# Kernel tuning notes

Hardware: AMD Instinct MI355X
Metric: run time of the kernel (lower is better)

Reference implementation:

```python
import jax, jax.numpy as jnp
import numpy as np

T = 28  # MAX_SENT_LEN
NEG_SLOPE = 0.02  # LeakyReLU slope


def gru_step(x, h, Wih, Whh, bih, bhh):
    # torch GRU/GRUCell gate math, gate order (r, z, n)
    gi = x @ Wih.T + bih
    gh = h @ Whh.T + bhh
    ir, iz, inn = jnp.split(gi, 3, axis=-1)
    hr, hz, hn = jnp.split(gh, 3, axis=-1)
    r = jax.nn.sigmoid(ir + hr)
    zg = jax.nn.sigmoid(iz + hz)
    n = jnp.tanh(inn + r * hn)
    return (1.0 - zg) * n + zg * h


def setup_inputs() -> dict:
    key = jax.random.key(0)
    ks = jax.random.split(key, 24)
    V, E, H, D, L, B = 32000, 256, 512, 512, 128, 512
    s = lambda i, shape: jax.random.normal(ks[i], shape, jnp.float32) * 0.05
    return dict(
        x=jax.random.randint(ks[0], (B, T), 0, V),
        x_lens=jax.random.randint(ks[1], (B,), 1, T + 1),  # lengths in [1, 28]
        emb=s(2, (V, E)),
        enc_Wih_f=s(3, (3 * H, E)), enc_Whh_f=s(4, (3 * H, H)),
        enc_bih_f=s(5, (3 * H,)), enc_bhh_f=s(6, (3 * H,)),
        enc_Wih_b=s(7, (3 * H, E)), enc_Whh_b=s(8, (3 * H, H)),
        enc_bih_b=s(9, (3 * H,)), enc_bhh_b=s(10, (3 * H,)),
        fc1_w=s(11, (L, 2 * H)), fc1_b=s(12, (L,)),
        fc2_w=s(13, (D, L)), fc2_b=s(14, (D,)),
        dec_Wih=s(15, (3 * D, D)), dec_Whh=s(16, (3 * D, D)),
        dec_bih=s(17, (3 * D,)), dec_bhh=s(18, (3 * D,)),
        re_w=s(19, (E, D)), re_b=s(20, (E,)),
        hv_w=s(21, (V, D)), hv_b=s(22, (V,)),
    )


def reference(x, x_lens, emb, enc_Wih_f, enc_Whh_f, enc_bih_f, enc_bhh_f,
              enc_Wih_b, enc_Whh_b, enc_bih_b, enc_bhh_b,
              fc1_w, fc1_b, fc2_w, fc2_b,
              dec_Wih, dec_Whh, dec_bih, dec_bhh,
              re_w, re_b, hv_w, hv_b):
    B = x.shape[0]
    H = enc_Whh_f.shape[1]
    embedded = emb[x]                       # [B,T,E]
    xs = jnp.swapaxes(embedded, 0, 1)       # [T,B,E]

    # forward direction of the packed bidirectional GRU: output at t=len-1
    # equals hidden after len steps (padding only affects later steps)
    def fstep(h, xt):
        hn = gru_step(xt, h, enc_Wih_f, enc_Whh_f, enc_bih_f, enc_bhh_f)
        return hn, hn
    h0 = jnp.zeros((B, H), embedded.dtype)
    _, ys = jax.lax.scan(fstep, h0, xs)     # [T,B,H]

    idx = x_lens - 1
    bidx = jnp.arange(B)
    ctx_f = jnp.swapaxes(ys, 0, 1)[bidx, idx]     # [B,H]
    # backward direction processes token len-1 first with h0=0, so its
    # output at position len-1 is a single GRU step on the last valid token
    x_last = embedded[bidx, idx]                  # [B,E]
    ctx_b = gru_step(x_last, h0, enc_Wih_b, enc_Whh_b, enc_bih_b, enc_bhh_b)
    context = jnp.concatenate([ctx_f, ctx_b], axis=-1)  # [B,2H]

    z = context @ fc1_w.T + fc1_b            # [B,latent]; dropout = identity (eval)

    # decoder: tf_prob=0 -> pure recurrence; same input fc_2(z) every step,
    # initial hidden = fc_2(z)
    out0 = z @ fc2_w.T + fc2_b                # [B,D]
    def dstep(h, _):
        hn = gru_step(out0, h, dec_Wih, dec_Whh, dec_bih, dec_bhh)
        return hn, hn
    _, outs = jax.lax.scan(dstep, out0, None, length=T)  # [T,B,D]

    re_emb = outs @ re_w.T + re_b             # [T,B,E]
    re_emb = jnp.where(re_emb >= 0, re_emb, NEG_SLOPE * re_emb)
    re_emb = jnp.swapaxes(re_emb, 0, 1)       # [B,T,E]
    logits = outs @ hv_w.T + hv_b             # [T,B,V]
    return logits, z, re_emb
```

## Files before the change

### kernel.cpp

```cpp
#include <hip/hip_runtime.h>

typedef unsigned short u16;
typedef unsigned int u32;
typedef __attribute__((ext_vector_type(8))) short bf16x8;
typedef __attribute__((ext_vector_type(4))) float f32x4;

#define GLOBAL_AS __attribute__((address_space(1)))
#define LDS_AS __attribute__((address_space(3)))

__device__ __forceinline__ float b2f(u16 u) {
    union { float f; u32 i; } v; v.i = ((u32)u) << 16; return v.f;
}
__device__ __forceinline__ u16 f2b(float f) {
    union { float f; u32 i; } v; v.f = f;
    u32 i = v.i;
    u32 r = (i + 0x7FFFu + ((i >> 16) & 1u)) >> 16;
    return (u16)r;
}
__device__ __forceinline__ float sigm(float x) { return 1.f / (1.f + expf(-x)); }

struct CvtJobs {
    const float* src[9];
    u16*         dst[9];
    int          end4[9];
};
__global__ void cvt_multi(CvtJobs jobs, int total4)
{
    for (int id = blockIdx.x * 256 + threadIdx.x; id < total4;
         id += gridDim.x * 256) {
        int s = 0;
        while (id >= jobs.end4[s]) ++s;
        int base = (s == 0) ? 0 : jobs.end4[s - 1];
        int i = id - base;
        float4 v = ((const float4*)jobs.src[s])[i];
        u32 w0 = (u32)f2b(v.x) | ((u32)f2b(v.y) << 16);
        u32 w1 = (u32)f2b(v.z) | ((u32)f2b(v.w) << 16);
        ((u32*)jobs.dst[s])[i * 2]     = w0;
        ((u32*)jobs.dst[s])[i * 2 + 1] = w1;
    }
}

template<bool LEAKY, bool REMAP>
__global__ __launch_bounds__(256)
void gemm_bt(const u16* __restrict__ A, const u16* __restrict__ W,
             const float* __restrict__ bias,
             float* __restrict__ Cf, u16* __restrict__ Cb,
             int M, int N, int K)
{
    __shared__ __align__(16) u16 lA[128 * 64];
    __shared__ __align__(16) u16 lB[128 * 64];

    const int tid  = threadIdx.x;
    const int lane = tid & 63;
    const int w    = tid >> 6;
    const int wr   = w >> 1;
    const int wc   = w & 1;
    const int m0   = blockIdx.y * 128;
    const int n0   = blockIdx.x * 128;

    const int lrow = lane & 15;
    const int kgrp = lane >> 4;

    f32x4 acc[4][4] = {};

    for (int k0 = 0; k0 < K; k0 += 64) {
        #pragma unroll
        for (int s = 0; s < 4; ++s) {
            int seg = w * 4 + s;
            int g   = seg * 64 + lane;
            int row = g >> 3;
            int kk  = (g & 7) * 8;
            const u16* gA = A + (size_t)(m0 + row) * K + k0 + kk;
            const u16* gB = W + (size_t)(n0 + row) * K + k0 + kk;
            __builtin_amdgcn_global_load_lds((GLOBAL_AS const void*)gA,
                                             (LDS_AS void*)(&lA[seg * 512]), 16, 0, 0);
            __builtin_amdgcn_global_load_lds((GLOBAL_AS const void*)gB,
                                             (LDS_AS void*)(&lB[seg * 512]), 16, 0, 0);
        }
        __syncthreads();
        #pragma unroll
        for (int kk = 0; kk < 64; kk += 32) {
            bf16x8 af[4], bfr[4];
            #pragma unroll
            for (int i = 0; i < 4; ++i) {
                int ar = wr * 64 + i * 16 + lrow;
                af[i]  = *(const bf16x8*)&lA[ar * 64 + kk + kgrp * 8];
                int br = wc * 64 + i * 16 + lrow;
                bfr[i] = *(const bf16x8*)&lB[br * 64 + kk + kgrp * 8];
            }
            #pragma unroll
            for (int mi = 0; mi < 4; ++mi)
                #pragma unroll
                for (int ni = 0; ni < 4; ++ni)
                    acc[mi][ni] = __builtin_amdgcn_mfma_f32_16x16x32_bf16(
                        af[mi], bfr[ni], acc[mi][ni], 0, 0, 0);
        }
        __syncthreads();
    }

    #pragma unroll
    for (int mi = 0; mi < 4; ++mi) {
        #pragma unroll
        for (int ni = 0; ni < 4; ++ni) {
            int gcol = n0 + wc * 64 + ni * 16 + lrow;
            float bv = bias ? bias[gcol] : 0.f;
            #pragma unroll
            for (int r = 0; r < 4; ++r) {
                int grow = m0 + wr * 64 + mi * 16 + kgrp * 4 + r;
                float v = acc[mi][ni][r] + bv;
                if (LEAKY) v = (v >= 0.f) ? v : 0.02f * v;
                size_t oidx;
                if (REMAP) {
                    int bb = grow & 511, tt = grow >> 9;
                    oidx = ((size_t)bb * 28 + tt) * (size_t)N + gcol;
                } else {
                    oidx = (size_t)grow * (size_t)N + gcol;
                }
                if (Cf) Cf[oidx] = v;
                if (Cb) Cb[oidx] = f2b(v);
            }
        }
    }
}

__global__ __launch_bounds__(512)
void gemm_logits(const u16* __restrict__ A, const u16* __restrict__ W,
                 const float* __restrict__ bias, float* __restrict__ C,
                 int M, int N)
{
    constexpr int K = 512;
    __shared__ __align__(16) u16 lds[4 * 2 * 8192];

    const int tid  = threadIdx.x;
    const int lane = tid & 63;
    const int w    = tid >> 6;
    const int wr   = w >> 2;
    const int wc   = w & 3;
    const int l15  = lane & 15;
    const int kg   = lane >> 4;

    {
    }
    int id = blockIdx.x;
    int xcd = id & 7;
    int o   = id >> 3;
    int g, r;
    if (o < 840) { g = o / 56; r = o % 56; }
    else         { g = 15;     r = o - 840; }
    const int by = xcd * 7 + (r % 7);
    const int bx = g * 8 + (r / 7);
    const int m0 = by * 256;
    const int n0 = bx * 256;

    auto stage = [&](int kt, int buf) {
        #pragma unroll
        for (int ld = 0; ld < 2; ++ld) {
            int g2  = ld * 512 + tid;
            int row = g2 >> 2;
            int cp  = g2 & 3;
            int scp = cp ^ ((row >> 1) & 3);
            const u16* sA = A + (size_t)(m0 + row) * K + kt * 32 + scp * 8;
            const u16* sB = W + (size_t)(n0 + row) * K + kt * 32 + scp * 8;
            u32 dst = (u32)buf * 32768u + (u32)(ld * 512 + w * 64) * 16u;
            __builtin_amdgcn_global_load_lds((GLOBAL_AS const void*)sA,
                (LDS_AS void*)((char*)lds + dst), 16, 0, 0);
            __builtin_amdgcn_global_load_lds((GLOBAL_AS const void*)sB,
                (LDS_AS void*)((char*)lds + dst + 16384u), 16, 0, 0);
        }
    };

    f32x4 acc[8][4] = {};

    auto compute = [&](int buf) {
        const char* base = (const char*)lds + buf * 32768;
        bf16x8 a[8], b[4];
        #pragma unroll
        for (int mi = 0; mi < 8; ++mi) {
            int rr = wr * 128 + mi * 16 + l15;
            a[mi] = *(const bf16x8*)(base + rr * 64 + ((kg ^ ((rr >> 1) & 3)) << 4));
        }
        #pragma unroll
        for (int ni = 0; ni < 4; ++ni) {
            int rr = wc * 64 + ni * 16 + l15;
            b[ni] = *(const bf16x8*)(base + 16384 + rr * 64 + ((kg ^ ((rr >> 1) & 3)) << 4));
        }
        __builtin_amdgcn_s_setprio(1);
        #pragma unroll
        for (int mi = 0; mi < 8; ++mi)
            #pragma unroll
            for (int ni = 0; ni < 4; ++ni)
                acc[mi][ni] = __builtin_amdgcn_mfma_f32_16x16x32_bf16(
                    a[mi], b[ni], acc[mi][ni], 0, 0, 0);
        __builtin_amdgcn_s_setprio(0);
    };

    stage(0, 0);
    stage(1, 1);
    stage(2, 2);

    #pragma unroll 1
    for (int kt = 0; kt < 13; ++kt) {
        asm volatile("s_waitcnt vmcnt(8)" ::: "memory");
        __builtin_amdgcn_sched_barrier(0);
        __builtin_amdgcn_s_barrier();
        asm volatile("" ::: "memory");
        __builtin_amdgcn_sched_barrier(0);
        stage(kt + 3, (kt + 3) & 3);
        compute(kt & 3);
    }
    asm volatile("s_waitcnt vmcnt(8)" ::: "memory");
    __builtin_amdgcn_sched_barrier(0);
    __builtin_amdgcn_s_barrier();
    asm volatile("" ::: "memory");
    __builtin_amdgcn_sched_barrier(0);
    compute(1);
    asm volatile("s_waitcnt vmcnt(4)" ::: "memory");
    __builtin_amdgcn_sched_barrier(0);
    __builtin_amdgcn_s_barrier();
    asm volatile("" ::: "memory");
    __builtin_amdgcn_sched_barrier(0);
    compute(2);
    asm volatile("s_waitcnt vmcnt(0)" ::: "memory");
    __builtin_amdgcn_sched_barrier(0);
    __builtin_amdgcn_s_barrier();
    asm volatile("" ::: "memory");
    __builtin_amdgcn_sched_barrier(0);
    compute(3);

    #pragma unroll
    for (int ni = 0; ni < 4; ++ni) {
        int gcol = n0 + wc * 64 + ni * 16 + l15;
        float bv = bias[gcol];
        #pragma unroll
        for (int mi = 0; mi < 8; ++mi) {
            #pragma unroll
            for (int r = 0; r < 4; ++r) {
                int grow = m0 + wr * 128 + mi * 16 + kg * 4 + r;
                __builtin_nontemporal_store(acc[mi][ni][r] + bv,
                                            &C[(size_t)grow * (size_t)N + gcol]);
            }
        }
    }
}

template<bool IS_DEC>
__global__ __launch_bounds__(256)
void scan_step(const u16* __restrict__ gi,
               const u16* __restrict__ Whh,
               const float* __restrict__ bhh,
               const u16* __restrict__ hprev_b,
               const float* __restrict__ hprev_f,
               u16* __restrict__ hnext_b,
               float* __restrict__ hnext_f,
               const int* __restrict__ xlens,
               u16* __restrict__ ctx,
               u16* __restrict__ outs,
               int t)
{
    __shared__ __align__(16) u16 lB[96 * 512];
    __shared__ __align__(16) u16 lA[32 * 512];

    const int tid  = threadIdx.x;
    const int lane = tid & 63;
    const int w    = tid >> 6;
    const int rh   = w >> 1;
    const int jh   = w & 1;
    const int bc   = blockIdx.x >> 4;
    const int jc   = blockIdx.x & 15;

    const int l15 = lane & 15;
    const int kg  = lane >> 4;

    #pragma unroll
    for (int s = 0; s < 24; ++s) {
        int g    = s * 256 + tid;
        int rr   = g >> 6;
        int cp   = g & 63;
        int gate = rr >> 5;
        int c    = rr & 31;
        int whrow = gate * 512 + jc * 32 + c;
        const u16* src = Whh + (size_t)whrow * 512 + (size_t)((cp ^ (rr & 7)) * 8);
        __builtin_amdgcn_global_load_lds((GLOBAL_AS const void*)src,
            (LDS_AS void*)((char*)lB + (s * 256 + w * 64) * 16), 16, 0, 0);
    }
    #pragma unroll
    for (int s = 0; s < 8; ++s) {
        int g   = s * 256 + tid;
        int row = g >> 6;
        int cp  = g & 63;
        const u16* src = hprev_b + (size_t)(bc * 32 + row) * 512
                                 + (size_t)((cp ^ (row & 7)) * 8);
        __builtin_amdgcn_global_load_lds((GLOBAL_AS const void*)src,
            (LDS_AS void*)((char*)lA + (s * 256 + w * 64) * 16), 16, 0, 0);
    }

    const int jloc = jh * 16 + l15;
    const int j    = jc * 32 + jloc;
    const int rowb = bc * 32 + rh * 16 + kg * 4;
    const float bhr = bhh[j], bhz = bhh[512 + j], bhn = bhh[1024 + j];

    const u16* gi_t = IS_DEC ? gi : gi + (size_t)t * 512 * 1536;
    float gir[4], giz[4], gin[4], hold[4];
    int   xl[4];
    #pragma unroll
    for (int r = 0; r < 4; ++r) {
        int row = rowb + r;
        gir[r]  = b2f(gi_t[row * 1536 + j]);
        giz[r]  = b2f(gi_t[row * 1536 + 512 + j]);
        gin[r]  = b2f(gi_t[row * 1536 + 1024 + j]);
        hold[r] = hprev_f[row * 512 + j];
        if (!IS_DEC) xl[r] = xlens[row];
    }
    __syncthreads();

    f32x4 acc[3] = {};
    const int arow = rh * 16 + l15;
    #pragma unroll 4
    for (int kc = 0; kc < 16; ++kc) {
        int k2 = kc * 64 + kg * 16;
        bf16x8 a = *(const bf16x8*)((const char*)lA + arow * 1024
                                    + (k2 ^ ((arow & 7) << 4)));
        #pragma unroll
        for (int g3 = 0; g3 < 3; ++g3) {
            int rr = g3 * 32 + jloc;
            bf16x8 b = *(const bf16x8*)((const char*)lB + rr * 1024
                                        + (k2 ^ ((rr & 7) << 4)));
            acc[g3] = __builtin_amdgcn_mfma_f32_16x16x32_bf16(a, b, acc[g3], 0, 0, 0);
        }
    }

    #pragma unroll
    for (int r = 0; r < 4; ++r) {
        int row = rowb + r;
        float rg = sigm(gir[r] + acc[0][r] + bhr);
        float zg = sigm(giz[r] + acc[1][r] + bhz);
        float ng = tanhf(gin[r] + rg * (acc[2][r] + bhn));
        float hn = (1.f - zg) * ng + zg * hold[r];
        hnext_f[row * 512 + j] = hn;
        hnext_b[row * 512 + j] = f2b(hn);
        if (IS_DEC) outs[((size_t)t * 512 + row) * 512 + j] = f2b(hn);
        else if (xl[r] - 1 == t) ctx[row * 1024 + j] = f2b(hn);
    }
}

__global__ void embed_k(const int* __restrict__ x, const int* __restrict__ xlens,
                        const float* __restrict__ emb,
                        u16* __restrict__ embedded, u16* __restrict__ x_last)
{
    int id = blockIdx.x * 256 + threadIdx.x;
    if (id >= 28 * 512 * 128) return;
    int e2 = id & 127;
    int tb = id >> 7;
    int b  = tb & 511;
    int t  = tb >> 9;
    int tok = x[b * 28 + t];
    const float* src = emb + (size_t)tok * 256 + e2 * 2;
    u32 v = (u32)f2b(src[0]) | ((u32)f2b(src[1]) << 16);
    *(u32*)(embedded + (size_t)tb * 256 + e2 * 2) = v;
    if (t == xlens[b] - 1)
        *(u32*)(x_last + (size_t)b * 256 + e2 * 2) = v;
}

__global__ void ctxb_k(const float* __restrict__ gi, const float* __restrict__ bhh,
                       u16* __restrict__ ctx)
{
    int idx = blockIdx.x * 256 + threadIdx.x;
    if (idx >= 512 * 512) return;
    int b = idx >> 9, j = idx & 511;
    int base = b * 1536;
    float r = sigm(gi[base + j] + bhh[j]);
    float z = sigm(gi[base + 512 + j] + bhh[512 + j]);
    float n = tanhf(gi[base + 1024 + j] + r * bhh[1024 + j]);
    ctx[b * 1024 + 512 + j] = f2b((1.f - z) * n);
}


extern "C" void kernel_launch(void* const* d_in, const int* in_sizes, int n_in,
                              void* d_out, int out_size, void* d_ws, size_t ws_size,
                              hipStream_t stream)
{
    const int*   x      = (const int*)d_in[0];
    const int*   xlens  = (const int*)d_in[1];
    const float* emb    = (const float*)d_in[2];
    const float* Wih_f  = (const float*)d_in[3];
    const float* Whh_f  = (const float*)d_in[4];
    const float* bih_f  = (const float*)d_in[5];
    const float* bhh_f  = (const float*)d_in[6];
    const float* Wih_b  = (const float*)d_in[7];
    const float* bih_b  = (const float*)d_in[9];
    const float* bhh_b  = (const float*)d_in[10];
    const float* fc1_w  = (const float*)d_in[11];
    const float* fc1_b  = (const float*)d_in[12];
    const float* fc2_w  = (const float*)d_in[13];
    const float* fc2_b  = (const float*)d_in[14];
    const float* dWih   = (const float*)d_in[15];
    const float* dWhh   = (const float*)d_in[16];
    const float* dbih   = (const float*)d_in[17];
    const float* dbhh   = (const float*)d_in[18];
    const float* re_w   = (const float*)d_in[19];
    const float* re_b   = (const float*)d_in[20];
    const float* hv_w   = (const float*)d_in[21];
    const float* hv_b   = (const float*)d_in[22];

    float* out        = (float*)d_out;
    float* out_logits = out;
    float* out_z      = out + (size_t)28 * 512 * 32000;
    float* out_re     = out_z + 512 * 128;

    char* ws = (char*)d_ws;
    size_t off = 0;
    auto alloc = [&](size_t bytes) -> void* {
        void* p = ws + off; off += (bytes + 255) & ~(size_t)255; return p;
    };
    u16* wWihf = (u16*)alloc(1536 * 256 * 2);
    u16* wWhhf = (u16*)alloc(1536 * 512 * 2);
    u16* wWihb = (u16*)alloc(1536 * 256 * 2);
    u16* wfc1  = (u16*)alloc(128 * 1024 * 2);
    u16* wfc2  = (u16*)alloc(512 * 128 * 2);
    u16* wdWih = (u16*)alloc(1536 * 512 * 2);
    u16* wdWhh = (u16*)alloc(1536 * 512 * 2);
    u16* wre   = (u16*)alloc(256 * 512 * 2);
    u16* whv   = (u16*)alloc((size_t)32000 * 512 * 2);
    u16*   hb0    = (u16*)  alloc(512 * 512 * 2);
    u16*   hb1    = (u16*)  alloc(512 * 512 * 2);
    float* hf0    = (float*)alloc(512 * 512 * 4);
    float* hf1    = (float*)alloc(512 * 512 * 4);
    u16*   ctx    = (u16*)  alloc(512 * 1024 * 2);
    float* gi_bw  = (float*)alloc(512 * 1536 * 4);
    u16*   out_zb = (u16*)  alloc(512 * 128 * 2);
    u16*   gi_dec = (u16*)  alloc(512 * 1536 * 2);
    u16*   outsb  = (u16*)  alloc((size_t)28 * 512 * 512 * 2);

    char* ds = (char*)d_out;
    size_t doff = 0;
    auto dalloc = [&](size_t bytes) -> void* {
        void* p = ds + doff; doff += (bytes + 255) & ~(size_t)255; return p;
    };
    u16* embedded = (u16*)dalloc((size_t)28 * 512 * 256 * 2);
    u16* x_last   = (u16*)dalloc(512 * 256 * 2);
    u16* gi_f     = (u16*)dalloc((size_t)28 * 512 * 1536 * 2);

    {
        CvtJobs jobs;
        const float* s[9] = { Wih_f, Whh_f, Wih_b, fc1_w, fc2_w, dWih, dWhh, re_w, hv_w };
        u16*         d[9] = { wWihf, wWhhf, wWihb, wfc1, wfc2, wdWih, wdWhh, wre, whv };
        int          n[9] = { 1536*256, 1536*512, 1536*256, 128*1024, 512*128,
                              1536*512, 1536*512, 256*512, 32000*512 };
        int cum = 0;
        for (int i = 0; i < 9; ++i) {
            jobs.src[i] = s[i]; jobs.dst[i] = d[i];
            cum += n[i] / 4; jobs.end4[i] = cum;
        }
        cvt_multi<<<2048, 256, 0, stream>>>(jobs, cum);
    }
    hipMemsetAsync(hb0, 0, 512 * 512 * 2, stream);
    hipMemsetAsync(hf0, 0, 512 * 512 * 4, stream);

    embed_k<<<7168, 256, 0, stream>>>(x, xlens, emb, embedded, x_last);

    gemm_bt<false, false><<<dim3(12, 112), 256, 0, stream>>>(
        embedded, wWihf, bih_f, nullptr, gi_f, 14336, 1536, 256);

    gemm_bt<false, false><<<dim3(12, 4), 256, 0, stream>>>(
        x_last, wWihb, bih_b, gi_bw, nullptr, 512, 1536, 256);
    ctxb_k<<<1024, 256, 0, stream>>>(gi_bw, bhh_b, ctx);

    {
        u16*   hb[2] = { hb0, hb1 };
        float* hf[2] = { hf0, hf1 };
        for (int t = 0; t < 28; ++t) {
            int s = t & 1, d = s ^ 1;
            scan_step<false><<<256, 256, 0, stream>>>(
                gi_f, wWhhf, bhh_f, hb[s], hf[s], hb[d], hf[d],
                xlens, ctx, nullptr, t);
        }
    }

    gemm_bt<false, false><<<dim3(1, 4), 256, 0, stream>>>(
        ctx, wfc1, fc1_b, out_z, out_zb, 512, 128, 1024);

    gemm_bt<false, false><<<dim3(4, 4), 256, 0, stream>>>(
        out_zb, wfc2, fc2_b, hf0, hb0, 512, 512, 128);

    gemm_bt<false, false><<<dim3(12, 4), 256, 0, stream>>>(
        hb0, wdWih, dbih, nullptr, gi_dec, 512, 1536, 512);

    {
        u16*   hb[2] = { hb0, hb1 };
        float* hf[2] = { hf0, hf1 };
        for (int t = 0; t < 28; ++t) {
            int s = t & 1, d = s ^ 1;
            scan_step<true><<<256, 256, 0, stream>>>(
                gi_dec, wdWhh, dbhh, hb[s], hf[s], hb[d], hf[d],
                nullptr, nullptr, outsb, t);
        }
    }

    gemm_bt<true, true><<<dim3(2, 112), 256, 0, stream>>>(
        outsb, wre, re_b, out_re, nullptr, 14336, 256, 512);

    gemm_logits<<<7000, 512, 0, stream>>>(
        outsb, whv, hv_b, out_logits, 14336, 32000);
}
```

Measured before the change: 1.152 ms.

## Shrink logits GEMM tile to 128x256 and read scan Whh directly from global

The logits GEMM moves from 256x256 tiles with a 4-stage LDS ring to 128x256 tiles with a 2-stage double buffer. This cuts LDS use and registers per block so more blocks fit per CU (launch bounds set to 4), and the grid doubles to 14000 blocks. The scan step kernel stops staging the Whh slice in LDS and loads B fragments straight from global memory (L2-cached), which removes the per-step LDS fill and its 96KB footprint. The costs are lower arithmetic intensity per tile in the GEMM and uncoalesced global reads in the scan inner loop.

```diff
diff --git a/kernel.cpp b/kernel.cpp
--- a/kernel.cpp
+++ b/kernel.cpp
@@ -123,13 +123,13 @@
     }
 }
 
-__global__ __launch_bounds__(512)
+__global__ __launch_bounds__(512, 4)
 void gemm_logits(const u16* __restrict__ A, const u16* __restrict__ W,
                  const float* __restrict__ bias, float* __restrict__ C,
                  int M, int N)
 {
     constexpr int K = 512;
-    __shared__ __align__(16) u16 lds[4 * 2 * 8192];
+    __shared__ __align__(16) u16 lds[2 * 12288];
 
     const int tid  = threadIdx.x;
     const int lane = tid & 63;
@@ -139,103 +139,87 @@
     const int l15  = lane & 15;
     const int kg   = lane >> 4;
 
-    {
-    }
-    int id = blockIdx.x;
+    int id  = blockIdx.x;
     int xcd = id & 7;
     int o   = id >> 3;
     int g, r;
-    if (o < 840) { g = o / 56; r = o % 56; }
-    else         { g = 15;     r = o - 840; }
-    const int by = xcd * 7 + (r % 7);
-    const int bx = g * 8 + (r / 7);
-    const int m0 = by * 256;
+    if (o < 1680) { g = o / 112; r = o % 112; }
+    else          { g = 15;      r = o - 1680; }
+    const int by = xcd * 14 + (r % 14);
+    const int bx = g * 8 + (r / 14);
+    const int m0 = by * 128;
     const int n0 = bx * 256;
 
     auto stage = [&](int kt, int buf) {
-        #pragma unroll
-        for (int ld = 0; ld < 2; ++ld) {
-            int g2  = ld * 512 + tid;
-            int row = g2 >> 2;
-            int cp  = g2 & 3;
+        {
+            int row = tid >> 2, cp = tid & 3;
             int scp = cp ^ ((row >> 1) & 3);
             const u16* sA = A + (size_t)(m0 + row) * K + kt * 32 + scp * 8;
-            const u16* sB = W + (size_t)(n0 + row) * K + kt * 32 + scp * 8;
-            u32 dst = (u32)buf * 32768u + (u32)(ld * 512 + w * 64) * 16u;
+            u32 dst = (u32)buf * 24576u + (u32)(w * 64) * 16u;
             __builtin_amdgcn_global_load_lds((GLOBAL_AS const void*)sA,
                 (LDS_AS void*)((char*)lds + dst), 16, 0, 0);
+        }
+        #pragma unroll
+        for (int ld = 0; ld < 2; ++ld) {
+            int gch = ld * 512 + tid;
+            int row = gch >> 2, cp = gch & 3;
+            int scp = cp ^ ((row >> 1) & 3);
+            const u16* sB = W + (size_t)(n0 + row) * K + kt * 32 + scp * 8;
+            u32 dst = (u32)buf * 24576u + 8192u + (u32)(ld * 512 + w * 64) * 16u;
             __builtin_amdgcn_global_load_lds((GLOBAL_AS const void*)sB,
-                (LDS_AS void*)((char*)lds + dst + 16384u), 16, 0, 0);
+                (LDS_AS void*)((char*)lds + dst), 16, 0, 0);
         }
     };
 
-    f32x4 acc[8][4] = {};
-
-    auto compute = [&](int buf) {
-        const char* base = (const char*)lds + buf * 32768;
-        bf16x8 a[8], b[4];
-        #pragma unroll
-        for (int mi = 0; mi < 8; ++mi) {
-            int rr = wr * 128 + mi * 16 + l15;
+    f32x4 acc[4][4] = {};
+
+    stage(0, 0);
+    stage(1, 1);
+
+    #pragma unroll 1
+    for (int kt = 0; kt < 16; ++kt) {
+        if (kt < 15) { asm volatile("s_waitcnt vmcnt(3)" ::: "memory"); }
+        else         { asm volatile("s_waitcnt vmcnt(0)" ::: "memory"); }
+        __builtin_amdgcn_sched_barrier(0);
+        __builtin_amdgcn_s_barrier();
+        asm volatile("" ::: "memory");
+        __builtin_amdgcn_sched_barrier(0);
+
+        const char* base = (const char*)lds + (kt & 1) * 24576;
+        bf16x8 a[4], b[4];
+        #pragma unroll
+        for (int mi = 0; mi < 4; ++mi) {
+            int rr = wr * 64 + mi * 16 + l15;
             a[mi] = *(const bf16x8*)(base + rr * 64 + ((kg ^ ((rr >> 1) & 3)) << 4));
         }
         #pragma unroll
         for (int ni = 0; ni < 4; ++ni) {
-            int rr = wc * 64 + ni * 16 + l15;
-            b[ni] = *(const bf16x8*)(base + 16384 + rr * 64 + ((kg ^ ((rr >> 1) & 3)) << 4));
+            int rb = wc * 64 + ni * 16 + l15;
+            b[ni] = *(const bf16x8*)(base + 8192 + rb * 64 + ((kg ^ ((rb >> 1) & 3)) << 4));
+        }
+        if (kt < 14) {
+            __syncthreads();
+            stage(kt + 2, kt & 1);
         }
         __builtin_amdgcn_s_setprio(1);
         #pragma unroll
-        for (int mi = 0; mi < 8; ++mi)
+        for (int mi = 0; mi < 4; ++mi)
             #pragma unroll
             for (int ni = 0; ni < 4; ++ni)
                 acc[mi][ni] = __builtin_amdgcn_mfma_f32_16x16x32_bf16(
                     a[mi], b[ni], acc[mi][ni], 0, 0, 0);
         __builtin_amdgcn_s_setprio(0);
-    };
-
-    stage(0, 0);
-    stage(1, 1);
-    stage(2, 2);
-
-    #pragma unroll 1
-    for (int kt = 0; kt < 13; ++kt) {
-        asm volatile("s_waitcnt vmcnt(8)" ::: "memory");
-        __builtin_amdgcn_sched_barrier(0);
-        __builtin_amdgcn_s_barrier();
-        asm volatile("" ::: "memory");
-        __builtin_amdgcn_sched_barrier(0);
-        stage(kt + 3, (kt + 3) & 3);
-        compute(kt & 3);
-    }
-    asm volatile("s_waitcnt vmcnt(8)" ::: "memory");
-    __builtin_amdgcn_sched_barrier(0);
-    __builtin_amdgcn_s_barrier();
-    asm volatile("" ::: "memory");
-    __builtin_amdgcn_sched_barrier(0);
-    compute(1);
-    asm volatile("s_waitcnt vmcnt(4)" ::: "memory");
-    __builtin_amdgcn_sched_barrier(0);
-    __builtin_amdgcn_s_barrier();
-    asm volatile("" ::: "memory");
-    __builtin_amdgcn_sched_barrier(0);
-    compute(2);
-    asm volatile("s_waitcnt vmcnt(0)" ::: "memory");
-    __builtin_amdgcn_sched_barrier(0);
-    __builtin_amdgcn_s_barrier();
-    asm volatile("" ::: "memory");
-    __builtin_amdgcn_sched_barrier(0);
-    compute(3);
+    }
 
     #pragma unroll
     for (int ni = 0; ni < 4; ++ni) {
         int gcol = n0 + wc * 64 + ni * 16 + l15;
         float bv = bias[gcol];
         #pragma unroll
-        for (int mi = 0; mi < 8; ++mi) {
+        for (int mi = 0; mi < 4; ++mi) {
             #pragma unroll
             for (int r = 0; r < 4; ++r) {
-                int grow = m0 + wr * 128 + mi * 16 + kg * 4 + r;
+                int grow = m0 + wr * 64 + mi * 16 + kg * 4 + r;
                 __builtin_nontemporal_store(acc[mi][ni][r] + bv,
                                             &C[(size_t)grow * (size_t)N + gcol]);
             }
@@ -257,7 +241,6 @@
                u16* __restrict__ outs,
                int t)
 {
-    __shared__ __align__(16) u16 lB[96 * 512];
     __shared__ __align__(16) u16 lA[32 * 512];
 
     const int tid  = threadIdx.x;
@@ -271,18 +254,6 @@
     const int l15 = lane & 15;
     const int kg  = lane >> 4;
 
-    #pragma unroll
-    for (int s = 0; s < 24; ++s) {
-        int g    = s * 256 + tid;
-        int rr   = g >> 6;
-        int cp   = g & 63;
-        int gate = rr >> 5;
-        int c    = rr & 31;
-        int whrow = gate * 512 + jc * 32 + c;
-        const u16* src = Whh + (size_t)whrow * 512 + (size_t)((cp ^ (rr & 7)) * 8);
-        __builtin_amdgcn_global_load_lds((GLOBAL_AS const void*)src,
-            (LDS_AS void*)((char*)lB + (s * 256 + w * 64) * 16), 16, 0, 0);
-    }
     #pragma unroll
     for (int s = 0; s < 8; ++s) {
         int g   = s * 256 + tid;
@@ -322,9 +293,8 @@
                                     + (k2 ^ ((arow & 7) << 4)));
         #pragma unroll
         for (int g3 = 0; g3 < 3; ++g3) {
-            int rr = g3 * 32 + jloc;
-            bf16x8 b = *(const bf16x8*)((const char*)lB + rr * 1024
-                                        + (k2 ^ ((rr & 7) << 4)));
+            const bf16x8 b = *(const bf16x8*)(Whh
+                + (size_t)(g3 * 512 + jc * 32 + jloc) * 512 + kc * 32 + kg * 8);
             acc[g3] = __builtin_amdgcn_mfma_f32_16x16x32_bf16(a, b, acc[g3], 0, 0, 0);
         }
     }
@@ -499,6 +469,6 @@
     gemm_bt<true, true><<<dim3(2, 112), 256, 0, stream>>>(
         outsb, wre, re_b, out_re, nullptr, 14336, 256, 512);
 
-    gemm_logits<<<7000, 512, 0, stream>>>(
+    gemm_logits<<<14000, 512, 0, stream>>>(
         outsb, whv, hv_b, out_logits, 14336, 32000);
 }
```

Result: slower. 1.259 ms (+9.3%).
